# Optimization experiments

Measured on AMD Instinct MI355X. Metric: run time of the kernel, lower is better.

## Reference

```python
import jax, jax.numpy as jnp
import numpy as np
from jax import lax

B, T, S = 64, 4096, 64


def setup_inputs() -> dict:
    key = jax.random.key(0)
    k1, k2, k3 = jax.random.split(key, 3)
    transition_potentials = jax.random.normal(k1, (S, S), dtype=jnp.float32)
    emission_potentials = jax.random.normal(k2, (B, T, S), dtype=jnp.float32)
    seq_lens = jax.random.randint(k3, (B,), 1, T + 1)
    return {
        "transition_potentials": transition_potentials,
        "emission_potentials": emission_potentials,
        "seq_lens": seq_lens,
    }


def reference(transition_potentials, emission_potentials, seq_lens):
    # potential_normalization='none', potential_scale=1.0 -> normalize is identity.
    # HMM forward algorithm: alpha[t] = logsumexp_i(alpha[t-1,i] + A[i,j]) + emis[t]
    alpha0 = emission_potentials[:, 0, :]  # [B,S]

    def step(alpha_prev, emis_t):
        # alpha_prev: [B,S]; emis_t: [B,S]; transition: [S,S]
        alpha_t = jax.nn.logsumexp(
            alpha_prev[:, :, None] + transition_potentials[None, :, :], axis=1
        ) + emis_t
        return alpha_t, alpha_t

    emis_rest = jnp.moveaxis(emission_potentials[:, 1:, :], 1, 0)  # [T-1,B,S]
    _, alphas = lax.scan(step, alpha0, emis_rest)  # [T-1,B,S]
    alpha = jnp.concatenate([alpha0[None], alphas], axis=0)  # [T,B,S]
    alpha = jnp.moveaxis(alpha, 0, 1)  # [B,T,S]
    log_Z = jax.nn.logsumexp(alpha[:, -1, :], axis=-1)  # [B]
    return alpha, log_Z
```

## Files before the change

### kernel.cpp

```cpp
#include <hip/hip_runtime.h>
#include <hip/hip_bf16.h>


#define BB 64
#define TT 4096
#define SS 64
#define C_CH 128
#define LL 32
#define WARM 24
#define PF 8
#define WSLAB 32768

typedef __attribute__((ext_vector_type(4))) short bh4;
typedef __attribute__((ext_vector_type(4))) float f32x4;
typedef __attribute__((ext_vector_type(4))) unsigned short us4;

#define LOG2E 1.44269504088896340736f
#define LN2F  0.69314718055994530942f

__device__ __forceinline__ float fexp2(float x) {
#if __has_builtin(__builtin_amdgcn_exp2f)
    return __builtin_amdgcn_exp2f(x);
#else
    return exp2f(x);
#endif
}
__device__ __forceinline__ float flog2(float x) {
#if __has_builtin(__builtin_amdgcn_logf)
    return __builtin_amdgcn_logf(x);
#else
    return log2f(x);
#endif
}
__device__ __forceinline__ int pack_bf16(float x, float y) {
    __hip_bfloat162 h = __float22bfloat162_rn(make_float2(x, y));
    int r; __builtin_memcpy(&r, &h, 4); return r;
}
__device__ __forceinline__ float bf_to_f32(unsigned short u) {
    unsigned int w = ((unsigned int)u) << 16;
    float f; __builtin_memcpy(&f, &w, 4); return f;
}
union PB2 { int i[2]; bh4 v; us4 u; };

__device__ __forceinline__ f32x4 mfma16(bh4 a, bh4 b, f32x4 c) {
#if __has_builtin(__builtin_amdgcn_mfma_f32_16x16x16bf16_1k)
    return __builtin_amdgcn_mfma_f32_16x16x16bf16_1k(a, b, c, 0, 0, 0);
#else
    asm("v_mfma_f32_16x16x16_bf16 %0, %1, %2, %0" : "+v"(c) : "v"(a), "v"(b));
    return c;
#endif
}

__device__ __forceinline__ void do_step(f32x4 (&vv)[4], const f32x4 (&eE)[4],
                                        const bh4 (&Af)[4][4]) {
    bh4 Bf[4];
    #pragma unroll
    for (int kb = 0; kb < 4; ++kb) {
        PB2 pb;
        pb.i[0] = pack_bf16(vv[kb].x, vv[kb].y);
        pb.i[1] = pack_bf16(vv[kb].z, vv[kb].w);
        Bf[kb] = pb.v;
    }
    #pragma unroll
    for (int jt = 0; jt < 4; ++jt) {
        f32x4 d0 = {0.f, 0.f, 0.f, 0.f};
        f32x4 d1 = {0.f, 0.f, 0.f, 0.f};
        d0 = mfma16(Af[jt][0], Bf[0], d0);
        d1 = mfma16(Af[jt][1], Bf[1], d1);
        d0 = mfma16(Af[jt][2], Bf[2], d0);
        d1 = mfma16(Af[jt][3], Bf[3], d1);
        f32x4 d = d0 + d1;
        vv[jt] = d * eE[jt];
    }
}

__device__ __forceinline__ void load_row(f32x4 (&dst)[4],
                                         const float* __restrict__ eb,
                                         int t, int off) {
    const float* p = eb + (t & (TT - 1)) * SS + off;
    #pragma unroll
    for (int jt = 0; jt < 4; ++jt)
        dst[jt] = *(const f32x4*)(p + 16 * jt);
}

__global__ __launch_bounds__(64)
__attribute__((amdgpu_waves_per_eu(1, 1)))
void hmm_phaseA(const float* __restrict__ trans,
                const float* __restrict__ emis,
                unsigned short* __restrict__ wsv,
                float* __restrict__ ws_warm,
                float* __restrict__ ws_bound) {
    const int lane = threadIdx.x;
    const int n = lane & 15, q = lane >> 4;
    const int w = blockIdx.x;
    const int b = w >> 3, cg = w & 7;
    const int c = 16 * cg + n;
    const bool is_c0 = (c == 0);
    const int off = 4 * q;

    bh4 Af[4][4];
    #pragma unroll
    for (int jt = 0; jt < 4; ++jt)
        #pragma unroll
        for (int kb = 0; kb < 4; ++kb) {
            float v0 = __expf(trans[(16 * kb + 4 * q + 0) * SS + 16 * jt + n]) * 0.015625f;
            float v1 = __expf(trans[(16 * kb + 4 * q + 1) * SS + 16 * jt + n]) * 0.015625f;
            float v2 = __expf(trans[(16 * kb + 4 * q + 2) * SS + 16 * jt + n]) * 0.015625f;
            float v3 = __expf(trans[(16 * kb + 4 * q + 3) * SS + 16 * jt + n]) * 0.015625f;
            PB2 pb;
            pb.i[0] = pack_bf16(v0, v1);
            pb.i[1] = pack_bf16(v2, v3);
            Af[jt][kb] = pb.v;
        }

    const float* eb = emis + (size_t)b * TT * SS;
    unsigned short* wslab = wsv + (size_t)w * WSLAB;

    const int t0 = LL * c - (WARM + 1);

    const float cL = is_c0 ? (-150.0f * LN2F) : 0.0f;

    f32x4 vv[4], e0v[4], ebuf[PF][4];
    {
        f32x4 a0[4], z0[4];
        load_row(a0, eb, t0, off);
        load_row(z0, eb, 0, off);
        #pragma unroll
        for (int jt = 0; jt < 4; ++jt) {
            vv[jt].x = fexp2(a0[jt].x * LOG2E);
            vv[jt].y = fexp2(a0[jt].y * LOG2E);
            vv[jt].z = fexp2(a0[jt].z * LOG2E);
            vv[jt].w = fexp2(a0[jt].w * LOG2E);
            e0v[jt].x = fexp2(z0[jt].x * LOG2E);
            e0v[jt].y = fexp2(z0[jt].y * LOG2E);
            e0v[jt].z = fexp2(z0[jt].z * LOG2E);
            e0v[jt].w = fexp2(z0[jt].w * LOG2E);
        }
    }
    #pragma unroll
    for (int k = 0; k < PF; ++k) load_row(ebuf[k], eb, t0 + 1 + k, off);

    #pragma unroll 1
    for (int g = 0; g < 3; ++g) {
        #pragma unroll
        for (int k = 0; k < PF; ++k) {
            int s = PF * g + k + 1;
            f32x4 eE[4];
            #pragma unroll
            for (int jt = 0; jt < 4; ++jt) {
                eE[jt].x = fexp2(ebuf[k][jt].x * LOG2E);
                eE[jt].y = fexp2(ebuf[k][jt].y * LOG2E);
                eE[jt].z = fexp2(ebuf[k][jt].z * LOG2E);
                eE[jt].w = fexp2(ebuf[k][jt].w * LOG2E);
            }
            load_row(ebuf[k], eb, t0 + s + PF, off);
            do_step(vv, eE, Af);
        }
    }
    if (lane < 16)
        ws_warm[b * C_CH + 16 * cg + lane] =
            fmaf(flog2(vv[0].x), LN2F, 144.0f * LN2F + cL);

    #pragma unroll 1
    for (int g = 0; g < 4; ++g) {
        #pragma unroll
        for (int k = 0; k < PF; ++k) {
            int s = WARM + 1 + PF * g + k;
            f32x4 eE[4];
            #pragma unroll
            for (int jt = 0; jt < 4; ++jt) {
                eE[jt].x = fexp2(ebuf[k][jt].x * LOG2E);
                eE[jt].y = fexp2(ebuf[k][jt].y * LOG2E);
                eE[jt].z = fexp2(ebuf[k][jt].z * LOG2E);
                eE[jt].w = fexp2(ebuf[k][jt].w * LOG2E);
            }
            load_row(ebuf[k], eb, t0 + s + PF, off);
            do_step(vv, eE, Af);
            if (k == 0 && g == 0 && is_c0) {
                #pragma unroll
                for (int jt = 0; jt < 4; ++jt) vv[jt] = e0v[jt];
            }
            unsigned short* wp = wslab + (n * 32 + (s - (WARM + 1))) * 64 + 4 * q;
            #pragma unroll
            for (int kb = 0; kb < 4; ++kb) {
                PB2 pb;
                pb.i[0] = pack_bf16(vv[kb].x, vv[kb].y);
                pb.i[1] = pack_bf16(vv[kb].z, vv[kb].w);
                *(us4*)(wp + 16 * kb) = pb.u;
            }
        }
    }
    if (lane < 16)
        ws_bound[b * C_CH + 16 * cg + lane] =
            fmaf(flog2(vv[0].x), LN2F, 336.0f * LN2F + cL);
}

__global__ __launch_bounds__(256)
void hmm_phaseC(float* __restrict__ out,
                const unsigned short* __restrict__ wsv,
                const float* __restrict__ ws_warm,
                const float* __restrict__ ws_bound) {
    const int b = blockIdx.x, c = blockIdx.y, tid = threadIdx.x;
    __shared__ float sd[C_CH];

    if (tid < C_CH) {
        float d = 0.f;
        if (tid > 0)
            d = ws_bound[b * C_CH + tid - 1] - ws_warm[b * C_CH + tid];
        sd[tid] = d;
    }
    __syncthreads();
    #pragma unroll
    for (int off = 1; off < C_CH; off <<= 1) {
        float v = 0.f;
        if (tid >= off && tid < C_CH) v = sd[tid - off];
        __syncthreads();
        if (tid >= off && tid < C_CH) sd[tid] += v;
        __syncthreads();
    }
    const float delta = sd[c];

    const int cg = c >> 4, n = c & 15;
    const unsigned short* src =
        wsv + (size_t)(b * 8 + cg) * WSLAB + n * 2048 + tid * 8;
    const int r = tid >> 3, col0 = (tid & 7) * 8;

    us4 u0 = *(const us4*)(src);
    us4 u1 = *(const us4*)(src + 4);

    const float cs = fmaf(6.0f * (float)(r + 25), LN2F,
                          (c == 0 ? -150.0f * LN2F : 0.0f) + delta);
    float a[8];
    #pragma unroll
    for (int i = 0; i < 4; ++i) {
        a[i]     = fmaf(flog2(bf_to_f32(u0[i])), LN2F, cs);
        a[4 + i] = fmaf(flog2(bf_to_f32(u1[i])), LN2F, cs);
    }

    float* dst = out + (size_t)b * TT * SS + (size_t)(32 * c + r) * SS + col0;
    *(f32x4*)(dst)     = *(f32x4*)&a[0];
    *(f32x4*)(dst + 4) = *(f32x4*)&a[4];

    if (c == C_CH - 1 && tid >= 248) {
        float mx = a[0];
        #pragma unroll
        for (int i = 1; i < 8; ++i) mx = fmaxf(mx, a[i]);
        #pragma unroll
        for (int off = 4; off >= 1; off >>= 1)
            mx = fmaxf(mx, __shfl_xor(mx, off, 64));
        float sv = 0.f;
        #pragma unroll
        for (int i = 0; i < 8; ++i) sv += __expf(a[i] - mx);
        #pragma unroll
        for (int off = 4; off >= 1; off >>= 1)
            sv += __shfl_xor(sv, off, 64);
        if (tid == 248)
            out[(size_t)BB * TT * SS + b] = mx + __logf(sv);
    }
}

extern "C" void kernel_launch(void* const* d_in, const int* in_sizes, int n_in,
                              void* d_out, int out_size, void* d_ws, size_t ws_size,
                              hipStream_t stream) {
    const float* trans = (const float*)d_in[0];
    const float* emis  = (const float*)d_in[1];
    float* out = (float*)d_out;

    float* ws_warm  = (float*)d_ws;
    float* ws_bound = ws_warm + BB * C_CH;
    unsigned short* wsv =
        (unsigned short*)(ws_bound + BB * C_CH);

    hmm_phaseA<<<dim3(BB * 8), dim3(64), 0, stream>>>(trans, emis, wsv,
                                                      ws_warm, ws_bound);
    hmm_phaseC<<<dim3(BB, C_CH), dim3(256), 0, stream>>>(out, wsv,
                                                         ws_warm, ws_bound);
}
```

Baseline: 146.2 us.

## Fuse HMM phases into one kernel with LDS history and inter-block flags

Merges the chunked forward-recursion kernel and the fix-up/output kernel into one launch. Each block keeps its bf16 alpha history in a 64KB XOR-swizzled LDS buffer instead of a global workspace. Blocks publish completion flags and spin-wait on earlier chunk groups of the same batch before doing a wave-level prefix scan of offsets and writing the outputs. This removes the global round-trip of the history and the second launch. In exchange it adds a memset, relies on co-residency of the 512 blocks to avoid deadlock, and reorders block-to-batch mapping so earlier chunk groups get scheduled first.

```diff
diff --git a/kernel.cpp b/kernel.cpp
--- a/kernel.cpp
+++ b/kernel.cpp
@@ -9,7 +9,6 @@
 #define LL 32
 #define WARM 24
 #define PF 8
-#define WSLAB 32768
 
 typedef __attribute__((ext_vector_type(4))) short bh4;
 typedef __attribute__((ext_vector_type(4))) float f32x4;
@@ -85,15 +84,19 @@
 
 __global__ __launch_bounds__(64)
 __attribute__((amdgpu_waves_per_eu(1, 1)))
-void hmm_phaseA(const float* __restrict__ trans,
-                const float* __restrict__ emis,
-                unsigned short* __restrict__ wsv,
-                float* __restrict__ ws_warm,
-                float* __restrict__ ws_bound) {
+void hmm_fused(const float* __restrict__ trans,
+               const float* __restrict__ emis,
+               float* __restrict__ out,
+               float* __restrict__ ws_warm,
+               float* __restrict__ ws_bound,
+               int* __restrict__ flags) {
+    __shared__ unsigned short hist[32768];
+
     const int lane = threadIdx.x;
     const int n = lane & 15, q = lane >> 4;
     const int w = blockIdx.x;
-    const int b = w >> 3, cg = w & 7;
+    const int b  = 8 * (w & 7) + ((w >> 3) & 7);
+    const int cg = w >> 6;
     const int c = 16 * cg + n;
     const bool is_c0 = (c == 0);
     const int off = 4 * q;
@@ -114,7 +117,6 @@
         }
 
     const float* eb = emis + (size_t)b * TT * SS;
-    unsigned short* wslab = wsv + (size_t)w * WSLAB;
 
     const int t0 = LL * c - (WARM + 1);
 
@@ -180,81 +182,85 @@
                 #pragma unroll
                 for (int jt = 0; jt < 4; ++jt) vv[jt] = e0v[jt];
             }
-            unsigned short* wp = wslab + (n * 32 + (s - (WARM + 1))) * 64 + 4 * q;
+            unsigned short* wp = hist + (n * 32 + (s - (WARM + 1))) * 64;
             #pragma unroll
             for (int kb = 0; kb < 4; ++kb) {
                 PB2 pb;
                 pb.i[0] = pack_bf16(vv[kb].x, vv[kb].y);
                 pb.i[1] = pack_bf16(vv[kb].z, vv[kb].w);
-                *(us4*)(wp + 16 * kb) = pb.u;
+                *(us4*)(wp + ((((kb << 2) + q) ^ n) << 2)) = pb.u;
             }
         }
     }
     if (lane < 16)
         ws_bound[b * C_CH + 16 * cg + lane] =
             fmaf(flog2(vv[0].x), LN2F, 336.0f * LN2F + cL);
-}
-
-__global__ __launch_bounds__(256)
-void hmm_phaseC(float* __restrict__ out,
-                const unsigned short* __restrict__ wsv,
-                const float* __restrict__ ws_warm,
-                const float* __restrict__ ws_bound) {
-    const int b = blockIdx.x, c = blockIdx.y, tid = threadIdx.x;
-    __shared__ float sd[C_CH];
-
-    if (tid < C_CH) {
-        float d = 0.f;
-        if (tid > 0)
-            d = ws_bound[b * C_CH + tid - 1] - ws_warm[b * C_CH + tid];
-        sd[tid] = d;
-    }
-    __syncthreads();
-    #pragma unroll
-    for (int off = 1; off < C_CH; off <<= 1) {
-        float v = 0.f;
-        if (tid >= off && tid < C_CH) v = sd[tid - off];
-        __syncthreads();
-        if (tid >= off && tid < C_CH) sd[tid] += v;
-        __syncthreads();
-    }
-    const float delta = sd[c];
-
-    const int cg = c >> 4, n = c & 15;
-    const unsigned short* src =
-        wsv + (size_t)(b * 8 + cg) * WSLAB + n * 2048 + tid * 8;
-    const int r = tid >> 3, col0 = (tid & 7) * 8;
-
-    us4 u0 = *(const us4*)(src);
-    us4 u1 = *(const us4*)(src + 4);
-
-    const float cs = fmaf(6.0f * (float)(r + 25), LN2F,
-                          (c == 0 ? -150.0f * LN2F : 0.0f) + delta);
-    float a[8];
-    #pragma unroll
-    for (int i = 0; i < 4; ++i) {
-        a[i]     = fmaf(flog2(bf_to_f32(u0[i])), LN2F, cs);
-        a[4 + i] = fmaf(flog2(bf_to_f32(u1[i])), LN2F, cs);
-    }
-
-    float* dst = out + (size_t)b * TT * SS + (size_t)(32 * c + r) * SS + col0;
-    *(f32x4*)(dst)     = *(f32x4*)&a[0];
-    *(f32x4*)(dst + 4) = *(f32x4*)&a[4];
-
-    if (c == C_CH - 1 && tid >= 248) {
-        float mx = a[0];
-        #pragma unroll
-        for (int i = 1; i < 8; ++i) mx = fmaxf(mx, a[i]);
-        #pragma unroll
-        for (int off = 4; off >= 1; off >>= 1)
-            mx = fmaxf(mx, __shfl_xor(mx, off, 64));
-        float sv = 0.f;
-        #pragma unroll
-        for (int i = 0; i < 8; ++i) sv += __expf(a[i] - mx);
-        #pragma unroll
-        for (int off = 4; off >= 1; off >>= 1)
-            sv += __shfl_xor(sv, off, 64);
-        if (tid == 248)
+
+    __threadfence();
+    if (lane == 0)
+        __hip_atomic_store(&flags[8 * b + cg], 1,
+                           __ATOMIC_RELEASE, __HIP_MEMORY_SCOPE_AGENT);
+    for (int p = 0; p < cg; ++p) {
+        while (__hip_atomic_load(&flags[8 * b + p],
+                                 __ATOMIC_ACQUIRE, __HIP_MEMORY_SCOPE_AGENT) == 0)
+            __builtin_amdgcn_s_sleep(8);
+    }
+    __threadfence();
+
+    const float* wwp = ws_warm + b * C_CH;
+    const float* wbp = ws_bound + b * C_CH;
+    float dlo = 0.f;
+    if (lane > 0) dlo = wbp[lane - 1] - wwp[lane];
+    float dhi = wbp[63 + lane] - wwp[64 + lane];
+    #pragma unroll
+    for (int o2 = 1; o2 < 64; o2 <<= 1) {
+        float v = __shfl_up(dlo, o2, 64);
+        if (lane >= o2) dlo += v;
+    }
+    #pragma unroll
+    for (int o2 = 1; o2 < 64; o2 <<= 1) {
+        float v = __shfl_up(dhi, o2, 64);
+        if (lane >= o2) dhi += v;
+    }
+    dhi += __shfl(dlo, 63, 64);
+
+    float* obase = out + (size_t)b * TT * SS + (size_t)(512 * cg) * SS;
+    const int lhi = lane >> 4, llo = lane & 15;
+    #pragma unroll 1
+    for (int nn = 0; nn < 16; ++nn) {
+        const int chunk = 16 * cg + nn;
+        const float dn = (chunk < 64) ? __shfl(dlo, chunk, 64)
+                                      : __shfl(dhi, chunk - 64, 64);
+        const float base_cs = (chunk == 0 ? -150.0f * LN2F : 0.0f) + dn;
+        #pragma unroll
+        for (int ii = 0; ii < 8; ++ii) {
+            const int r = ii * 4 + lhi;
+            const us4 u0 = *(const us4*)&hist[nn * 2048 + r * 64 +
+                                             ((llo ^ nn) << 2)];
+            const float cs = fmaf(6.0f * (float)(r + 25), LN2F, base_cs);
+            f32x4 a;
+            a.x = fmaf(flog2(bf_to_f32(u0[0])), LN2F, cs);
+            a.y = fmaf(flog2(bf_to_f32(u0[1])), LN2F, cs);
+            a.z = fmaf(flog2(bf_to_f32(u0[2])), LN2F, cs);
+            a.w = fmaf(flog2(bf_to_f32(u0[3])), LN2F, cs);
+            *(f32x4*)(obase + nn * 2048 + ii * 256 + lhi * 64 + llo * 4) = a;
+        }
+    }
+
+    if (cg == 7) {
+        const float d127 = __shfl(dhi, 63, 64);
+        const unsigned short hv =
+            hist[15 * 2048 + 31 * 64 + (((lane >> 2) ^ 15) << 2) + (lane & 3)];
+        float a = fmaf(flog2(bf_to_f32(hv)), LN2F, 336.0f * LN2F + d127);
+        float mx = a;
+        #pragma unroll
+        for (int o2 = 32; o2 >= 1; o2 >>= 1)
+            mx = fmaxf(mx, __shfl_xor(mx, o2, 64));
+        float sv = __expf(a - mx);
+        #pragma unroll
+        for (int o2 = 32; o2 >= 1; o2 >>= 1)
+            sv += __shfl_xor(sv, o2, 64);
+        if (lane == 0)
             out[(size_t)BB * TT * SS + b] = mx + __logf(sv);
     }
 }
@@ -268,11 +274,9 @@
 
     float* ws_warm  = (float*)d_ws;
     float* ws_bound = ws_warm + BB * C_CH;
-    unsigned short* wsv =
-        (unsigned short*)(ws_bound + BB * C_CH);
-
-    hmm_phaseA<<<dim3(BB * 8), dim3(64), 0, stream>>>(trans, emis, wsv,
-                                                      ws_warm, ws_bound);
-    hmm_phaseC<<<dim3(BB, C_CH), dim3(256), 0, stream>>>(out, wsv,
-                                                         ws_warm, ws_bound);
-}
+    int*   flags    = (int*)(ws_bound + BB * C_CH);
+
+    hipMemsetAsync(flags, 0, BB * 8 * sizeof(int), stream);
+    hmm_fused<<<dim3(BB * 8), dim3(64), 0, stream>>>(trans, emis, out,
+                                                     ws_warm, ws_bound, flags);
+}
```

Result: slower. 186.0 us (+27.2%).
